# Optimization experiments

Hardware: AMD Instinct MI355X
Metric: run time of the kernel (lower is better)

The kernel has to match this reference:

```python
import jax, jax.numpy as jnp
import numpy as np

B, L, H = 4, 2048, 1024
NQ, NKV, D = 8, 2, 256
I, V = 3584, 16384
EPS = 1e-6
THETA = 1e7
ROPE_DIM = 64

def rmsnorm(x, w, eps=EPS):
    xf = x.astype(jnp.float32)
    rms = jax.lax.rsqrt(jnp.mean(xf * xf, axis=-1, keepdims=True) + eps)
    return (xf * rms).astype(x.dtype) * w

def apply_rope(x, positions):
    # x: [B, H, L, D]; rotate first ROPE_DIM dims, interleaved pairs
    n_pairs = ROPE_DIM // 2
    inv_freq = THETA ** (-2.0 * jnp.arange(n_pairs, dtype=jnp.float32) / ROPE_DIM)
    freqs = positions.astype(jnp.float32)[:, None] * inv_freq[None, :]  # [L, n_pairs]
    cos = jnp.cos(freqs)[None, None, :, :]
    sin = jnp.sin(freqs)[None, None, :, :]
    b, h, l, d = x.shape
    xr = x[..., :ROPE_DIM].reshape(b, h, l, n_pairs, 2)
    x0, x1 = xr[..., 0], xr[..., 1]
    r0 = x0 * cos - x1 * sin
    r1 = x0 * sin + x1 * cos
    rotated = jnp.stack([r0, r1], axis=-1).reshape(b, h, l, ROPE_DIM)
    return jnp.concatenate([rotated, x[..., ROPE_DIM:]], axis=-1)

def setup_inputs() -> dict:
    key = jax.random.key(0)
    ks = jax.random.split(key, 12)
    s = 0.02
    return {
        "embeddings": jax.random.normal(ks[0], (B, L, H), jnp.float32),
        "hidden_states": jax.random.normal(ks[1], (B, L, H), jnp.float32),
        "pre_emb_w": jnp.ones((H,), jnp.float32),
        "pre_hid_w": jnp.ones((H,), jnp.float32),
        "fc_w": jax.random.normal(ks[2], (H, 2 * H), jnp.float32) * s,
        "in_ln_w": jnp.ones((H,), jnp.float32),
        "q_w": jax.random.normal(ks[3], (2 * NQ * D, H), jnp.float32) * s,
        "k_w": jax.random.normal(ks[4], (NKV * D, H), jnp.float32) * s,
        "v_w": jax.random.normal(ks[5], (NKV * D, H), jnp.float32) * s,
        "o_w": jax.random.normal(ks[6], (H, NQ * D), jnp.float32) * s,
        "qn_w": jnp.ones((D,), jnp.float32),
        "kn_w": jnp.ones((D,), jnp.float32),
        "post_ln_w": jnp.ones((H,), jnp.float32),
        "gate_w": jax.random.normal(ks[7], (I, H), jnp.float32) * s,
        "up_w": jax.random.normal(ks[8], (I, H), jnp.float32) * s,
        "down_w": jax.random.normal(ks[9], (H, I), jnp.float32) * s,
        "norm_w": jnp.ones((H,), jnp.float32),
        "lm_w": jax.random.normal(ks[10], (V, H), jnp.float32) * s,
    }

def _attention(x, q_w, k_w, v_w, o_w, qn_w, kn_w):
    b, l, _ = x.shape
    qg = (x @ q_w.T).reshape(b, l, NQ, 2, D)
    q = qg[:, :, :, 0, :]
    gate = qg[:, :, :, 1, :]
    k = (x @ k_w.T).reshape(b, l, NKV, D)
    v = (x @ v_w.T).reshape(b, l, NKV, D)
    q = rmsnorm(q, qn_w)
    k = rmsnorm(k, kn_w)
    groups = NQ // NKV
    k = jnp.repeat(k, groups, axis=2)  # [B, L, NQ, D]
    v = jnp.repeat(v, groups, axis=2)
    q, k, v = (t.transpose(0, 2, 1, 3) for t in (q, k, v))  # [B, NQ, L, D]
    positions = jnp.arange(l)
    q = apply_rope(q, positions)
    k = apply_rope(k, positions)
    scores = jnp.einsum('bhqd,bhkd->bhqk', q, k) / jnp.sqrt(jnp.float32(D))
    causal = jnp.tril(jnp.ones((l, l), jnp.bool_))
    scores = jnp.where(causal[None, None], scores, jnp.finfo(scores.dtype).min)
    attn = jax.nn.softmax(scores, axis=-1)
    out = jnp.einsum('bhqk,bhkd->bhqd', attn, v)
    out = out.transpose(0, 2, 1, 3).reshape(b, l, NQ * D)
    out = out * jax.nn.sigmoid(gate.reshape(b, l, NQ * D))
    return out @ o_w.T

def reference(embeddings, hidden_states, pre_emb_w, pre_hid_w, fc_w, in_ln_w,
              q_w, k_w, v_w, o_w, qn_w, kn_w, post_ln_w, gate_w, up_w, down_w,
              norm_w, lm_w):
    x = jnp.concatenate([rmsnorm(embeddings, pre_emb_w),
                         rmsnorm(hidden_states, pre_hid_w)], axis=-1)
    x = x @ fc_w.T
    residual = x
    x = rmsnorm(x, in_ln_w)
    x = _attention(x, q_w, k_w, v_w, o_w, qn_w, kn_w)
    x = residual + x
    residual = x
    x = rmsnorm(x, post_ln_w)
    x = (jax.nn.silu(x @ gate_w.T) * (x @ up_w.T)) @ down_w.T
    x = residual + x
    x = rmsnorm(x, norm_w)
    return x @ lm_w.T
```

## Files before the change

### kernel.cpp

```cpp
#include <hip/hip_runtime.h>

typedef __bf16 bf16;
typedef __bf16 bf16x8 __attribute__((ext_vector_type(8)));
typedef __bf16 bf16x4 __attribute__((ext_vector_type(4)));
typedef float f32x4 __attribute__((ext_vector_type(4)));

__device__ inline f32x4 mfma16(bf16x8 a, bf16x8 b, f32x4 c) {
    return __builtin_amdgcn_mfma_f32_16x16x32_bf16(a, b, c, 0, 0, 0);
}

__device__ __forceinline__ void async_cp16(const void* g, void* l) {
    __builtin_amdgcn_global_load_lds(
        (__attribute__((address_space(1))) char*)g,
        (__attribute__((address_space(3))) char*)l,
        16, 0, 0);
}

__global__ __launch_bounds__(256) void w2b_kernel(const float* __restrict__ s,
                                                  bf16* __restrict__ d)
{
    const size_t i = ((size_t)blockIdx.x * 256 + threadIdx.x) * 4;
    const float4 f = *(const float4*)(s + i);
    bf16x4 t;
    t[0] = (bf16)f.x; t[1] = (bf16)f.y; t[2] = (bf16)f.z; t[3] = (bf16)f.w;
    *(bf16x4*)(d + i) = t;
}

template <int EPI>
__global__ __launch_bounds__(256) void gemm_kernel(
    const bf16* __restrict__ A, const bf16* __restrict__ B,
    const float* __restrict__ res, float* __restrict__ Cout,
    int M, int N, int K)
{
    __shared__ bf16 As[128 * 32];
    __shared__ bf16 Bs[128 * 32];
    const int tid = threadIdx.x;
    const int wave = tid >> 6, lane = tid & 63;
    const int quad = lane >> 4, l16 = lane & 15;

    const int nby = M >> 7, nbx = N >> 7;
    const int nwg = nbx * nby;
    int bid = blockIdx.x;
    {
        const int q = nwg >> 3, r = nwg & 7;
        const int x = bid & 7, loc = bid >> 3;
        bid = (x < r ? x * (q + 1) : r * (q + 1) + (x - r) * q) + loc;
    }
    const int pg = nbx << 3;
    const int g = bid / pg, rem = bid - g * pg;
    const int by = (g << 3) + (rem & 7);
    const int bx = rem >> 3;
    const int row0 = by << 7, col0 = bx << 7;
    const int wrow = ((wave >> 1) << 6), wcol = ((wave & 1) << 6);

    f32x4 acc[4][4] = {};

    const bf16* Ag = A + (size_t)(row0 + (tid >> 2)) * K + (tid & 3) * 8;
    const bf16* Bg = B + (size_t)(col0 + (tid >> 2)) * K + (tid & 3) * 8;
    bf16* Asw = As + wave * 512;
    bf16* Bsw = Bs + wave * 512;
    const size_t K64 = (size_t)64 * K;

    for (int kb = 0; kb < K; kb += 32) {
        async_cp16(Ag + kb,        Asw);
        async_cp16(Ag + K64 + kb,  Asw + 2048);
        async_cp16(Bg + kb,        Bsw);
        async_cp16(Bg + K64 + kb,  Bsw + 2048);
        __syncthreads();
        bf16x8 af[4], bfr[4];
#pragma unroll
        for (int i = 0; i < 4; ++i)
            af[i] = *(const bf16x8*)(&As[(wrow + i * 16 + l16) * 32 + quad * 8]);
#pragma unroll
        for (int j = 0; j < 4; ++j)
            bfr[j] = *(const bf16x8*)(&Bs[(wcol + j * 16 + l16) * 32 + quad * 8]);
#pragma unroll
        for (int i = 0; i < 4; ++i)
#pragma unroll
            for (int j = 0; j < 4; ++j)
                acc[i][j] = mfma16(af[i], bfr[j], acc[i][j]);
        __syncthreads();
    }

#pragma unroll
    for (int i = 0; i < 4; ++i) {
        const int row = row0 + wrow + i * 16 + quad * 4;
#pragma unroll
        for (int j = 0; j < 4; ++j) {
            const int col = col0 + wcol + j * 16 + l16;
#pragma unroll
            for (int r = 0; r < 4; ++r) {
                const size_t idx = (size_t)(row + r) * N + col;
                float v = acc[i][j][r];
                if (EPI == 1) Cout[idx] = v + res[idx];
                else          Cout[idx] = v;
            }
        }
    }
}

template <int EPI>
__global__ __launch_bounds__(512, 2) void gemm256_kernel(
    const bf16* __restrict__ A, const bf16* __restrict__ B,
    const float* __restrict__ res, float* __restrict__ Cout,
    int M, int N, int K)
{
    __shared__ bf16 As[2][2][128][64];
    __shared__ bf16 Bs[2][2][128][64];
    const int tid = threadIdx.x;
    const int wid = tid >> 6, lane = tid & 63;
    const int quad = lane >> 4, l16 = lane & 15;
    const int wm = wid >> 2, wn = wid & 3;
    const int xsw = l16 & 7;

    const int nby = M >> 8, nbx = N >> 8;
    const int nwg = nbx * nby;
    int bid = blockIdx.x;
    {
        const int q = nwg >> 3, r = nwg & 7;
        const int x = bid & 7, loc = bid >> 3;
        bid = (x < r ? x * (q + 1) : r * (q + 1) + (x - r) * q) + loc;
    }
    const int pg = nbx << 3;
    const int g = bid / pg, rem = bid - g * pg;
    const int by = (g << 3) + (rem & 7);
    const int bx = rem >> 3;
    const int row0 = by << 8, col0 = bx << 8;

    const int srow = tid >> 3;
    const int scol = ((tid & 7) ^ ((tid >> 3) & 7)) * 8;
    const bf16* Abase = A + (size_t)(row0 + srow) * K + scol;
    const bf16* Bbase = B + (size_t)(col0 + srow) * K + scol;
    const size_t K64 = (size_t)K * 64;
    const size_t K128 = (size_t)K * 128;

    f32x4 acc[8][4] = {};

#define STG_A(BUF, HH, KB) do { \
    const bf16* _g = Abase + (size_t)(HH) * K128 + (KB); \
    bf16* _l = &As[BUF][HH][0][0] + wid * 512; \
    async_cp16(_g, _l); \
    async_cp16(_g + K64, _l + 4096); } while (0)
#define STG_B(BUF, HH, KB) do { \
    const bf16* _g = Bbase + (size_t)(HH) * K128 + (KB); \
    bf16* _l = &Bs[BUF][HH][0][0] + wid * 512; \
    async_cp16(_g, _l); \
    async_cp16(_g + K64, _l + 4096); } while (0)

#define READ_A(RH) do { \
    _Pragma("unroll") for (int f = 0; f < 4; ++f) { \
        af[f*2+0] = *(const bf16x8*)(&Ah[(RH)*64 + f*16 + l16][(quad ^ xsw) * 8]); \
        af[f*2+1] = *(const bf16x8*)(&Ah[(RH)*64 + f*16 + l16][((4 + quad) ^ xsw) * 8]); } } while (0)

#define READ_B(CH, BF) do { \
    _Pragma("unroll") for (int f = 0; f < 2; ++f) { \
        BF[f*2+0] = *(const bf16x8*)(&Bh[bofs + (CH)*32 + f*16 + l16][(quad ^ xsw) * 8]); \
        BF[f*2+1] = *(const bf16x8*)(&Bh[bofs + (CH)*32 + f*16 + l16][((4 + quad) ^ xsw) * 8]); } } while (0)

#define MFMA_Q(RH, CH, BF) do { \
    _Pragma("unroll") for (int f = 0; f < 4; ++f) \
    _Pragma("unroll") for (int f2 = 0; f2 < 2; ++f2) { \
        acc[(RH)*4+f][(CH)*2+f2] = mfma16(af[f*2+0], BF[f2*2+0], acc[(RH)*4+f][(CH)*2+f2]); \
        acc[(RH)*4+f][(CH)*2+f2] = mfma16(af[f*2+1], BF[f2*2+1], acc[(RH)*4+f][(CH)*2+f2]); } } while (0)

    const int NT = K >> 6;
    STG_B(0, 0, 0); STG_B(0, 1, 0); STG_A(0, 0, 0); STG_A(0, 1, 0);
    if (NT > 1) {
        STG_B(1, 0, 64); STG_B(1, 1, 64); STG_A(1, 0, 64);
        asm volatile("s_waitcnt vmcnt(6)" ::: "memory");
    } else {
        asm volatile("s_waitcnt vmcnt(0)" ::: "memory");
    }
    __builtin_amdgcn_s_barrier();

    bf16x8 af[8], bf0[4], bf1[4];
    for (int t = 0; t < NT; ++t) {
        const int c = t & 1, n = c ^ 1;
        const bf16 (*Ah)[64] = As[c][wm];
        const bf16 (*Bh)[64] = Bs[c][wn >> 1];
        const int bofs = (wn & 1) * 64;
        const int kb1 = (t + 1) << 6, kb2 = (t + 2) << 6;
        READ_A(0); READ_B(0, bf0);
        if (t + 1 < NT) STG_A(n, 1, kb1);
        __builtin_amdgcn_s_barrier();
        asm volatile("s_waitcnt lgkmcnt(0)" ::: "memory");
        __builtin_amdgcn_sched_barrier(0);
        __builtin_amdgcn_s_setprio(1);
        MFMA_Q(0, 0, bf0);
        __builtin_amdgcn_s_setprio(0);
        __builtin_amdgcn_s_barrier();
        READ_B(1, bf1);
        if (t + 2 < NT) STG_B(c, 0, kb2);
        __builtin_amdgcn_s_barrier();
        asm volatile("s_waitcnt lgkmcnt(0)" ::: "memory");
        __builtin_amdgcn_sched_barrier(0);
        __builtin_amdgcn_s_setprio(1);
        MFMA_Q(0, 1, bf1);
        __builtin_amdgcn_s_setprio(0);
        __builtin_amdgcn_s_barrier();
        READ_A(1);
        if (t + 2 < NT) STG_B(c, 1, kb2);
        __builtin_amdgcn_s_barrier();
        asm volatile("s_waitcnt lgkmcnt(0)" ::: "memory");
        __builtin_amdgcn_sched_barrier(0);
        __builtin_amdgcn_s_setprio(1);
        MFMA_Q(1, 0, bf0);
        __builtin_amdgcn_s_setprio(0);
        __builtin_amdgcn_s_barrier();
        if (t + 2 < NT) STG_A(c, 0, kb2);
        __builtin_amdgcn_s_barrier();
        __builtin_amdgcn_s_setprio(1);
        MFMA_Q(1, 1, bf1);
        __builtin_amdgcn_s_setprio(0);
        if (t + 2 < NT)      { asm volatile("s_waitcnt vmcnt(6)" ::: "memory"); }
        else if (t + 1 < NT) { asm volatile("s_waitcnt vmcnt(0)" ::: "memory"); }
        __builtin_amdgcn_s_barrier();
    }
#undef STG_A
#undef STG_B
#undef READ_A
#undef READ_B
#undef MFMA_Q

#pragma unroll
    for (int fr = 0; fr < 8; ++fr) {
        const int row = row0 + wm * 128 + fr * 16 + quad * 4;
#pragma unroll
        for (int fc = 0; fc < 4; ++fc) {
            const int col = col0 + wn * 64 + fc * 16 + l16;
#pragma unroll
            for (int r = 0; r < 4; ++r) {
                const size_t idx = (size_t)(row + r) * N + col;
                float v = acc[fr][fc][r];
                if (EPI == 1) Cout[idx] = v + res[idx];
                else          Cout[idx] = v;
            }
        }
    }
}

__global__ __launch_bounds__(256) void prenorm_kernel(
    const float* __restrict__ emb, const float* __restrict__ hid,
    const float* __restrict__ we, const float* __restrict__ wh,
    bf16* __restrict__ xcat)
{
    const int rr = blockIdx.x * 4 + (threadIdx.x >> 6);
    const int lane = threadIdx.x & 63;
    const int half = rr & 1, row = rr >> 1;
    const float* x = (half ? hid : emb) + (size_t)row * 1024;
    const float* w = half ? wh : we;
    float4 v[4]; float ss = 0.f;
#pragma unroll
    for (int j = 0; j < 4; ++j) {
        v[j] = *(const float4*)(x + (size_t)(lane + 64 * j) * 4);
        ss += v[j].x * v[j].x + v[j].y * v[j].y + v[j].z * v[j].z + v[j].w * v[j].w;
    }
#pragma unroll
    for (int m = 32; m; m >>= 1) ss += __shfl_xor(ss, m, 64);
    const float rms = rsqrtf(ss * (1.f / 1024.f) + 1e-6f);
    bf16* o = xcat + (size_t)row * 2048 + half * 1024;
#pragma unroll
    for (int j = 0; j < 4; ++j) {
        const int d = (lane + 64 * j) * 4;
        float4 wv = *(const float4*)(w + d);
        bf16x4 t;
        t[0] = (bf16)(v[j].x * rms * wv.x);
        t[1] = (bf16)(v[j].y * rms * wv.y);
        t[2] = (bf16)(v[j].z * rms * wv.z);
        t[3] = (bf16)(v[j].w * rms * wv.w);
        *(bf16x4*)(o + d) = t;
    }
}

__global__ __launch_bounds__(256) void rmsnorm_kernel(
    const float* __restrict__ xin, const float* __restrict__ w, bf16* __restrict__ out)
{
    const int row = blockIdx.x * 4 + (threadIdx.x >> 6);
    const int lane = threadIdx.x & 63;
    const float* x = xin + (size_t)row * 1024;
    float4 v[4]; float ss = 0.f;
#pragma unroll
    for (int j = 0; j < 4; ++j) {
        v[j] = *(const float4*)(x + (size_t)(lane + 64 * j) * 4);
        ss += v[j].x * v[j].x + v[j].y * v[j].y + v[j].z * v[j].z + v[j].w * v[j].w;
    }
#pragma unroll
    for (int m = 32; m; m >>= 1) ss += __shfl_xor(ss, m, 64);
    const float rms = rsqrtf(ss * (1.f / 1024.f) + 1e-6f);
    bf16* o = out + (size_t)row * 1024;
#pragma unroll
    for (int j = 0; j < 4; ++j) {
        const int d = (lane + 64 * j) * 4;
        float4 wv = *(const float4*)(w + d);
        bf16x4 t;
        t[0] = (bf16)(v[j].x * rms * wv.x);
        t[1] = (bf16)(v[j].y * rms * wv.y);
        t[2] = (bf16)(v[j].z * rms * wv.z);
        t[3] = (bf16)(v[j].w * rms * wv.w);
        *(bf16x4*)(o + d) = t;
    }
}

__global__ __launch_bounds__(256) void qprep_kernel(
    const float* __restrict__ qg, const float* __restrict__ qn_w, bf16* __restrict__ qa)
{
    const int row = blockIdx.x * 4 + (threadIdx.x >> 6);
    const int lane = threadIdx.x & 63;
    const int h = row & 7, bl = row >> 3;
    const int l = bl & 2047, b = bl >> 11;
    const float* x = qg + (size_t)row * 512;
    float v[4]; float ss = 0.f;
#pragma unroll
    for (int j = 0; j < 4; ++j) { v[j] = x[lane + 64 * j]; ss += v[j] * v[j]; }
#pragma unroll
    for (int m = 32; m; m >>= 1) ss += __shfl_xor(ss, m, 64);
    const float rms = rsqrtf(ss * (1.f / 256.f) + 1e-6f);
    float y[4];
#pragma unroll
    for (int j = 0; j < 4; ++j) y[j] = v[j] * rms * qn_w[lane + 64 * j];
    {
        const float p = __shfl_xor(y[0], 1, 64);
        const int i2 = lane >> 1;
        const float inv = powf(1e7f, -(float)(2 * i2) * (1.f / 64.f));
        const float ang = (float)l * inv;
        const float c = cosf(ang), s = sinf(ang);
        y[0] = (lane & 1) ? (p * s + y[0] * c) : (y[0] * c - p * s);
    }
    bf16* o = qa + ((size_t)((b * 8 + h) * 2048 + l)) * 256;
#pragma unroll
    for (int j = 0; j < 4; ++j) o[lane + 64 * j] = (bf16)(y[j] * 0.0625f);
}

__global__ __launch_bounds__(256) void kprep_kernel(
    const float* __restrict__ kf, const float* __restrict__ kn_w, bf16* __restrict__ ka)
{
    const int row = blockIdx.x * 4 + (threadIdx.x >> 6);
    const int lane = threadIdx.x & 63;
    const int kv = row & 1, bl = row >> 1;
    const int l = bl & 2047, b = bl >> 11;
    const float* x = kf + (size_t)row * 256;
    float v[4]; float ss = 0.f;
#pragma unroll
    for (int j = 0; j < 4; ++j) { v[j] = x[lane + 64 * j]; ss += v[j] * v[j]; }
#pragma unroll
    for (int m = 32; m; m >>= 1) ss += __shfl_xor(ss, m, 64);
    const float rms = rsqrtf(ss * (1.f / 256.f) + 1e-6f);
    float y[4];
#pragma unroll
    for (int j = 0; j < 4; ++j) y[j] = v[j] * rms * kn_w[lane + 64 * j];
    {
        const float p = __shfl_xor(y[0], 1, 64);
        const int i2 = lane >> 1;
        const float inv = powf(1e7f, -(float)(2 * i2) * (1.f / 64.f));
        const float ang = (float)l * inv;
        const float c = cosf(ang), s = sinf(ang);
        y[0] = (lane & 1) ? (p * s + y[0] * c) : (y[0] * c - p * s);
    }
    bf16* o = ka + ((size_t)((b * 2 + kv) * 2048 + l)) * 256;
#pragma unroll
    for (int j = 0; j < 4; ++j) o[lane + 64 * j] = (bf16)y[j];
}

__global__ __launch_bounds__(256) void vprep_kernel(const float* __restrict__ vf,
                                                    bf16* __restrict__ vt)
{
    __shared__ float t[64][65];
    const int l0 = blockIdx.x << 6;
    const int d0 = blockIdx.y << 6;
    const int b = blockIdx.z >> 1, kv = blockIdx.z & 1;
    const int tx = threadIdx.x & 63, ty = threadIdx.x >> 6;
    const float* src = vf + ((size_t)b * 4096 + kv) * 256;
#pragma unroll
    for (int j = 0; j < 16; ++j) {
        const int l = ty + j * 4;
        t[l][tx] = src[(size_t)(l0 + l) * 512 + d0 + tx];
    }
    __syncthreads();
    bf16* dst = vt + (size_t)(b * 2 + kv) * 256 * 2048;
#pragma unroll
    for (int j = 0; j < 16; ++j) {
        const int d = ty + j * 4;
        dst[(size_t)(d0 + d) * 2048 + l0 + tx] = (bf16)t[tx][d];
    }
}

__global__ __launch_bounds__(256) void attn_kernel(
    const bf16* __restrict__ qa, const bf16* __restrict__ ka,
    const bf16* __restrict__ vt, float* __restrict__ of)
{
    __shared__ bf16 Ks[32 * 264];
    __shared__ bf16 Vt[256 * 40];
    __shared__ bf16 Pw[4 * 16 * 40];
    const int tid = threadIdx.x;
    const int wave = tid >> 6, lane = tid & 63;
    const int quad = lane >> 4, l16 = lane & 15;
    const int bid = blockIdx.x;
    const int j = bid & 15, h = (bid >> 4) & 7, b = bid >> 7;
    const int kvh = h >> 2;
    const bf16* qptr = qa + ((size_t)(b * 8 + h)) * 2048 * 256;
    const bf16* kptr = ka + ((size_t)(b * 2 + kvh)) * 2048 * 256;
    const bf16* vptr = vt + ((size_t)(b * 2 + kvh)) * 256 * 2048;
    float* optr = of + ((size_t)(b * 8 + h)) * 2048 * 256;

    for (int s = 0; s < 2; ++s) {
        const int qt = s ? (31 - j) : j;
        const int qbase = qt * 64 + wave * 16;

        bf16x8 qf[8];
#pragma unroll
        for (int db = 0; db < 8; ++db)
            qf[db] = *(const bf16x8*)(qptr + (size_t)(qbase + l16) * 256 + db * 32 + quad * 8);

        f32x4 o_acc[16] = {};
        float m_i[4], l_i[4];
#pragma unroll
        for (int r = 0; r < 4; ++r) { m_i[r] = -1e30f; l_i[r] = 0.f; }

        const int ntiles = qt * 2 + 2;
        for (int kt = 0; kt < ntiles; ++kt) {
            const int kvs = kt * 32;
#pragma unroll
            for (int c = 0; c < 4; ++c) {
                const int idx = tid + c * 256;
                const int kr = idx >> 5, kc = (idx & 31) * 8;
                *(bf16x8*)(&Ks[kr * 264 + kc]) = *(const bf16x8*)(kptr + (size_t)(kvs + kr) * 256 + kc);
                const int vd = idx >> 2, vc = (idx & 3) * 8;
                *(bf16x8*)(&Vt[vd * 40 + vc]) = *(const bf16x8*)(vptr + (size_t)vd * 2048 + kvs + vc);
            }
            __syncthreads();

            f32x4 s0 = {}, s1 = {};
#pragma unroll
            for (int db = 0; db < 8; ++db) {
                bf16x8 k0 = *(const bf16x8*)(&Ks[l16 * 264 + db * 32 + quad * 8]);
                bf16x8 k1 = *(const bf16x8*)(&Ks[(16 + l16) * 264 + db * 32 + quad * 8]);
                s0 = mfma16(qf[db], k0, s0);
                s1 = mfma16(qf[db], k1, s1);
            }

            float alpha[4], p0v[4], p1v[4];
#pragma unroll
            for (int r = 0; r < 4; ++r) {
                const int qrow = qbase + quad * 4 + r;
                float a0 = (kvs + l16 > qrow) ? -1e30f : s0[r];
                float a1 = (kvs + 16 + l16 > qrow) ? -1e30f : s1[r];
                float mx = fmaxf(a0, a1);
#pragma unroll
                for (int m = 8; m; m >>= 1) mx = fmaxf(mx, __shfl_xor(mx, m, 64));
                const float mnew = fmaxf(m_i[r], mx);
                const float a = __expf(m_i[r] - mnew);
                const float p0 = __expf(a0 - mnew);
                const float p1 = __expf(a1 - mnew);
                float ps = p0 + p1;
#pragma unroll
                for (int m = 8; m; m >>= 1) ps += __shfl_xor(ps, m, 64);
                l_i[r] = l_i[r] * a + ps;
                m_i[r] = mnew;
                alpha[r] = a; p0v[r] = p0; p1v[r] = p1;
            }
#pragma unroll
            for (int t = 0; t < 16; ++t) {
                f32x4 o = o_acc[t];
                o[0] *= alpha[0]; o[1] *= alpha[1]; o[2] *= alpha[2]; o[3] *= alpha[3];
                o_acc[t] = o;
            }
            bf16* pw = &Pw[wave * 16 * 40];
#pragma unroll
            for (int r = 0; r < 4; ++r) {
                pw[(quad * 4 + r) * 40 + l16]      = (bf16)p0v[r];
                pw[(quad * 4 + r) * 40 + 16 + l16] = (bf16)p1v[r];
            }
            __syncthreads();
            const bf16x8 pa = *(const bf16x8*)(&pw[l16 * 40 + quad * 8]);
#pragma unroll
            for (int t = 0; t < 16; ++t) {
                bf16x8 vfr = *(const bf16x8*)(&Vt[(t * 16 + l16) * 40 + quad * 8]);
                o_acc[t] = mfma16(pa, vfr, o_acc[t]);
            }
            __syncthreads();
        }

#pragma unroll
        for (int r = 0; r < 4; ++r) {
            const float inv = 1.f / l_i[r];
            const int row = qbase + quad * 4 + r;
#pragma unroll
            for (int t = 0; t < 16; ++t)
                optr[(size_t)row * 256 + t * 16 + l16] = o_acc[t][r] * inv;
        }
    }
}

__global__ void gating_kernel(const float* __restrict__ of, const float* __restrict__ qg,
                              bf16* __restrict__ ag)
{
    const size_t i = (size_t)blockIdx.x * 256 + threadIdx.x;
    const int d = (int)(i & 255);
    const int h = (int)((i >> 8) & 7);
    const size_t bl = i >> 11;
    const float o = of[((size_t)((bl >> 11) * 8 + h) * 2048 + (bl & 2047)) * 256 + d];
    const float g = qg[(bl * 8 + h) * 512 + 256 + d];
    ag[i] = (bf16)(o * (1.f / (1.f + __expf(-g))));
}

__global__ void silu_kernel(const float* __restrict__ g, const float* __restrict__ u,
                            bf16* __restrict__ h)
{
    const size_t i = ((size_t)blockIdx.x * 256 + threadIdx.x) * 4;
    const float4 gv = *(const float4*)(g + i);
    const float4 uv = *(const float4*)(u + i);
    bf16x4 t;
    t[0] = (bf16)(gv.x * (1.f / (1.f + __expf(-gv.x))) * uv.x);
    t[1] = (bf16)(gv.y * (1.f / (1.f + __expf(-gv.y))) * uv.y);
    t[2] = (bf16)(gv.z * (1.f / (1.f + __expf(-gv.z))) * uv.z);
    t[3] = (bf16)(gv.w * (1.f / (1.f + __expf(-gv.w))) * uv.w);
    *(bf16x4*)(h + i) = t;
}

extern "C" void kernel_launch(void* const* d_in, const int* in_sizes, int n_in,
                              void* d_out, int out_size, void* d_ws, size_t ws_size,
                              hipStream_t stream)
{
    const float* emb       = (const float*)d_in[0];
    const float* hid       = (const float*)d_in[1];
    const float* pre_emb_w = (const float*)d_in[2];
    const float* pre_hid_w = (const float*)d_in[3];
    const float* fc_w      = (const float*)d_in[4];
    const float* in_ln_w   = (const float*)d_in[5];
    const float* q_w       = (const float*)d_in[6];
    const float* k_w       = (const float*)d_in[7];
    const float* v_w       = (const float*)d_in[8];
    const float* o_w       = (const float*)d_in[9];
    const float* qn_w      = (const float*)d_in[10];
    const float* kn_w      = (const float*)d_in[11];
    const float* post_ln_w = (const float*)d_in[12];
    const float* gate_w    = (const float*)d_in[13];
    const float* up_w      = (const float*)d_in[14];
    const float* down_w    = (const float*)d_in[15];
    const float* norm_w    = (const float*)d_in[16];
    const float* lm_w      = (const float*)d_in[17];
    float* out = (float*)d_out;
    char* ws = (char*)d_ws;

    float* xres = (float*)(ws + 0);
    bf16*  xln  = (bf16*)(ws + 33554432);
    char*  C    = ws + 50331648;
    char*  D    = ws + 184549376;
    char*  E    = ws + 318767104;
    float* qg   = (float*)C;
    float* gf   = (float*)C;
    bf16*  xcat = (bf16*)D;
    float* kf   = (float*)(D + 33554432);
    float* vf   = (float*)(D + 50331648);
    float* of   = (float*)(D + 67108864);
    float* uf   = (float*)D;
    bf16*  qa   = (bf16*)E;
    bf16*  ka   = (bf16*)(E + 33554432);
    bf16*  va   = (bf16*)(E + 41943040);
    bf16*  ag   = (bf16*)E;
    bf16*  hb   = (bf16*)E;
    bf16*  wbC  = (bf16*)C;
    bf16*  wbD  = (bf16*)D;
    bf16*  wbDt = (bf16*)(D + 117440512);

    prenorm_kernel<<<4096, 256, 0, stream>>>(emb, hid, pre_emb_w, pre_hid_w, xcat);

    w2b_kernel<<<2048, 256, 0, stream>>>(fc_w, wbC);
    gemm_kernel<0><<<512, 256, 0, stream>>>(xcat, wbC, nullptr, xres, 8192, 1024, 2048);
    rmsnorm_kernel<<<2048, 256, 0, stream>>>(xres, in_ln_w, xln);

    w2b_kernel<<<4096, 256, 0, stream>>>(q_w, wbD);
    gemm256_kernel<0><<<512, 512, 0, stream>>>(xln, wbD, nullptr, qg, 8192, 4096, 1024);
    w2b_kernel<<<512, 256, 0, stream>>>(k_w, wbD);
    gemm_kernel<0><<<256, 256, 0, stream>>>(xln, wbD, nullptr, kf, 8192, 512, 1024);
    w2b_kernel<<<512, 256, 0, stream>>>(v_w, wbD);
    gemm_kernel<0><<<256, 256, 0, stream>>>(xln, wbD, nullptr, vf, 8192, 512, 1024);

    qprep_kernel<<<16384, 256, 0, stream>>>(qg, qn_w, qa);
    kprep_kernel<<<4096, 256, 0, stream>>>(kf, kn_w, ka);
    vprep_kernel<<<dim3(32, 4, 8), 256, 0, stream>>>(vf, va);
    attn_kernel<<<512, 256, 0, stream>>>(qa, ka, va, of);
    gating_kernel<<<65536, 256, 0, stream>>>(of, qg, ag);

    w2b_kernel<<<2048, 256, 0, stream>>>(o_w, wbC);
    gemm_kernel<1><<<512, 256, 0, stream>>>(ag, wbC, xres, xres, 8192, 1024, 2048);
    rmsnorm_kernel<<<2048, 256, 0, stream>>>(xres, post_ln_w, xln);

    w2b_kernel<<<3584, 256, 0, stream>>>(gate_w, wbDt);
    gemm256_kernel<0><<<448, 512, 0, stream>>>(xln, wbDt, nullptr, gf, 8192, 3584, 1024);
    w2b_kernel<<<3584, 256, 0, stream>>>(up_w, wbDt);
    gemm256_kernel<0><<<448, 512, 0, stream>>>(xln, wbDt, nullptr, uf, 8192, 3584, 1024);
    silu_kernel<<<28672, 256, 0, stream>>>(gf, uf, hb);

    w2b_kernel<<<3584, 256, 0, stream>>>(down_w, wbC);
    gemm_kernel<1><<<512, 256, 0, stream>>>(hb, wbC, xres, xres, 8192, 1024, 3584);
    rmsnorm_kernel<<<2048, 256, 0, stream>>>(xres, norm_w, xln);

    w2b_kernel<<<16384, 256, 0, stream>>>(lm_w, wbC);
    gemm256_kernel<0><<<2048, 512, 0, stream>>>(xln, wbC, nullptr, out, 8192, 16384, 1024);
}
```

Baseline: 1.880 ms.

## Prefetch next K/V tile into registers in attention and reschedule GEMM B reads

The attention kernel now loads the next K/V tile from global memory into registers while the current tile's QK and PV MFMAs run, then writes it to LDS after the tile finishes. This hides global load latency behind compute. The 256-tile GEMM now reads the first B fragment for the next k-step at the end of the current iteration and groups both B staging copies into one slot, changing how LDS reads and async copies overlap. The cost is higher register pressure in attention (8 extra bf16x8 per thread) and a changed LDS hazard ordering in the GEMM.

```diff
diff --git a/kernel.cpp b/kernel.cpp
--- a/kernel.cpp
+++ b/kernel.cpp
@@ -112,6 +112,7 @@
     const int quad = lane >> 4, l16 = lane & 15;
     const int wm = wid >> 2, wn = wid & 3;
     const int xsw = l16 & 7;
+    const int bofs = (wn & 1) * 64;
 
     const int nby = M >> 8, nbx = N >> 8;
     const int nwg = nbx * nby;
@@ -152,10 +153,10 @@
         af[f*2+0] = *(const bf16x8*)(&Ah[(RH)*64 + f*16 + l16][(quad ^ xsw) * 8]); \
         af[f*2+1] = *(const bf16x8*)(&Ah[(RH)*64 + f*16 + l16][((4 + quad) ^ xsw) * 8]); } } while (0)
 
-#define READ_B(CH, BF) do { \
+#define READ_Bp(BP, CH, BF) do { \
     _Pragma("unroll") for (int f = 0; f < 2; ++f) { \
-        BF[f*2+0] = *(const bf16x8*)(&Bh[bofs + (CH)*32 + f*16 + l16][(quad ^ xsw) * 8]); \
-        BF[f*2+1] = *(const bf16x8*)(&Bh[bofs + (CH)*32 + f*16 + l16][((4 + quad) ^ xsw) * 8]); } } while (0)
+        BF[f*2+0] = *(const bf16x8*)(&BP[bofs + (CH)*32 + f*16 + l16][(quad ^ xsw) * 8]); \
+        BF[f*2+1] = *(const bf16x8*)(&BP[bofs + (CH)*32 + f*16 + l16][((4 + quad) ^ xsw) * 8]); } } while (0)
 
 #define MFMA_Q(RH, CH, BF) do { \
     _Pragma("unroll") for (int f = 0; f < 4; ++f) \
@@ -174,13 +175,16 @@
     __builtin_amdgcn_s_barrier();
 
     bf16x8 af[8], bf0[4], bf1[4];
+    {
+        const bf16 (*Bh0)[64] = Bs[0][wn >> 1];
+        READ_Bp(Bh0, 0, bf0);
+    }
     for (int t = 0; t < NT; ++t) {
         const int c = t & 1, n = c ^ 1;
         const bf16 (*Ah)[64] = As[c][wm];
         const bf16 (*Bh)[64] = Bs[c][wn >> 1];
-        const int bofs = (wn & 1) * 64;
         const int kb1 = (t + 1) << 6, kb2 = (t + 2) << 6;
-        READ_A(0); READ_B(0, bf0);
+        READ_A(0);
         if (t + 1 < NT) STG_A(n, 1, kb1);
         __builtin_amdgcn_s_barrier();
         asm volatile("s_waitcnt lgkmcnt(0)" ::: "memory");
@@ -189,8 +193,7 @@
         MFMA_Q(0, 0, bf0);
         __builtin_amdgcn_s_setprio(0);
         __builtin_amdgcn_s_barrier();
-        READ_B(1, bf1);
-        if (t + 2 < NT) STG_B(c, 0, kb2);
+        READ_Bp(Bh, 1, bf1);
         __builtin_amdgcn_s_barrier();
         asm volatile("s_waitcnt lgkmcnt(0)" ::: "memory");
         __builtin_amdgcn_sched_barrier(0);
@@ -199,7 +202,7 @@
         __builtin_amdgcn_s_setprio(0);
         __builtin_amdgcn_s_barrier();
         READ_A(1);
-        if (t + 2 < NT) STG_B(c, 1, kb2);
+        if (t + 2 < NT) { STG_B(c, 0, kb2); STG_B(c, 1, kb2); }
         __builtin_amdgcn_s_barrier();
         asm volatile("s_waitcnt lgkmcnt(0)" ::: "memory");
         __builtin_amdgcn_sched_barrier(0);
@@ -214,12 +217,16 @@
         __builtin_amdgcn_s_setprio(0);
         if (t + 2 < NT)      { asm volatile("s_waitcnt vmcnt(6)" ::: "memory"); }
         else if (t + 1 < NT) { asm volatile("s_waitcnt vmcnt(0)" ::: "memory"); }
+        if (t + 1 < NT) {
+            const bf16 (*Bn_)[64] = Bs[n][wn >> 1];
+            READ_Bp(Bn_, 0, bf0);
+        }
         __builtin_amdgcn_s_barrier();
     }
 #undef STG_A
 #undef STG_B
 #undef READ_A
-#undef READ_B
+#undef READ_Bp
 #undef MFMA_Q
 
 #pragma unroll
@@ -417,17 +424,31 @@
         for (int r = 0; r < 4; ++r) { m_i[r] = -1e30f; l_i[r] = 0.f; }
 
         const int ntiles = qt * 2 + 2;
+#pragma unroll
+        for (int c = 0; c < 4; ++c) {
+            const int idx = tid + c * 256;
+            const int kr = idx >> 5, kc = (idx & 31) * 8;
+            *(bf16x8*)(&Ks[kr * 264 + kc]) = *(const bf16x8*)(kptr + (size_t)kr * 256 + kc);
+            const int vd = idx >> 2, vc = (idx & 3) * 8;
+            *(bf16x8*)(&Vt[vd * 40 + vc]) = *(const bf16x8*)(vptr + (size_t)vd * 2048 + vc);
+        }
+        __syncthreads();
+
         for (int kt = 0; kt < ntiles; ++kt) {
             const int kvs = kt * 32;
-#pragma unroll
-            for (int c = 0; c < 4; ++c) {
-                const int idx = tid + c * 256;
-                const int kr = idx >> 5, kc = (idx & 31) * 8;
-                *(bf16x8*)(&Ks[kr * 264 + kc]) = *(const bf16x8*)(kptr + (size_t)(kvs + kr) * 256 + kc);
-                const int vd = idx >> 2, vc = (idx & 3) * 8;
-                *(bf16x8*)(&Vt[vd * 40 + vc]) = *(const bf16x8*)(vptr + (size_t)vd * 2048 + kvs + vc);
-            }
-            __syncthreads();
+            const bool pf = (kt + 1 < ntiles);
+            bf16x8 kreg[4], vreg[4];
+            if (pf) {
+                const int kvs1 = kvs + 32;
+#pragma unroll
+                for (int c = 0; c < 4; ++c) {
+                    const int idx = tid + c * 256;
+                    const int kr = idx >> 5, kc = (idx & 31) * 8;
+                    kreg[c] = *(const bf16x8*)(kptr + (size_t)(kvs1 + kr) * 256 + kc);
+                    const int vd = idx >> 2, vc = (idx & 3) * 8;
+                    vreg[c] = *(const bf16x8*)(vptr + (size_t)vd * 2048 + kvs1 + vc);
+                }
+            }
 
             f32x4 s0 = {}, s1 = {};
 #pragma unroll
@@ -478,6 +499,18 @@
                 o_acc[t] = mfma16(pa, vfr, o_acc[t]);
             }
             __syncthreads();
+
+            if (pf) {
+#pragma unroll
+                for (int c = 0; c < 4; ++c) {
+                    const int idx = tid + c * 256;
+                    const int kr = idx >> 5, kc = (idx & 31) * 8;
+                    *(bf16x8*)(&Ks[kr * 264 + kc]) = kreg[c];
+                    const int vd = idx >> 2, vc = (idx & 3) * 8;
+                    *(bf16x8*)(&Vt[vd * 40 + vc]) = vreg[c];
+                }
+                __syncthreads();
+            }
         }
 
 #pragma unroll
```

After: 1.921 ms. 2.2% more time.

## Restructure GEMM main loop to prefetch next tile's LDS fragments and cut barriers

Applied to the files above, without the earlier changes.

The 256x256 bf16 GEMM main loop is rescheduled. The A fragments and both B fragment sets for the next K-tile are now read from LDS at the end of the current iteration, so the next iteration's MFMAs can start right away. Global-to-LDS staging is regrouped: both A halves are staged early and both B halves after the mid-iteration barrier. This cuts the workgroup barriers per K-step from about eight to two and uses partial lgkmcnt/vmcnt waits. The aim is to reduce barrier stalls and LDS latency exposure between MFMA batches, at the cost of more live fragment registers and a tighter buffer-reuse ordering that must stay race-free.

```diff
diff --git a/kernel.cpp b/kernel.cpp
--- a/kernel.cpp
+++ b/kernel.cpp
@@ -112,6 +112,7 @@
     const int quad = lane >> 4, l16 = lane & 15;
     const int wm = wid >> 2, wn = wid & 3;
     const int xsw = l16 & 7;
+    const int bofs = (wn & 1) * 64;
 
     const int nby = M >> 8, nbx = N >> 8;
     const int nwg = nbx * nby;
@@ -135,6 +136,7 @@
     const size_t K128 = (size_t)K * 128;
 
     f32x4 acc[8][4] = {};
+    bf16x8 af[8], bf0[4], bf1[4];
 
 #define STG_A(BUF, HH, KB) do { \
     const bf16* _g = Abase + (size_t)(HH) * K128 + (KB); \
@@ -147,15 +149,17 @@
     async_cp16(_g, _l); \
     async_cp16(_g + K64, _l + 4096); } while (0)
 
-#define READ_A(RH) do { \
+#define RD_A(BUF, RH) do { \
+    const bf16 (*Ah_)[64] = As[BUF][wm]; \
     _Pragma("unroll") for (int f = 0; f < 4; ++f) { \
-        af[f*2+0] = *(const bf16x8*)(&Ah[(RH)*64 + f*16 + l16][(quad ^ xsw) * 8]); \
-        af[f*2+1] = *(const bf16x8*)(&Ah[(RH)*64 + f*16 + l16][((4 + quad) ^ xsw) * 8]); } } while (0)
-
-#define READ_B(CH, BF) do { \
+        af[f*2+0] = *(const bf16x8*)(&Ah_[(RH)*64 + f*16 + l16][(quad ^ xsw) * 8]); \
+        af[f*2+1] = *(const bf16x8*)(&Ah_[(RH)*64 + f*16 + l16][((4 + quad) ^ xsw) * 8]); } } while (0)
+
+#define RD_B(BUF, CH, BF) do { \
+    const bf16 (*Bh_)[64] = Bs[BUF][wn >> 1]; \
     _Pragma("unroll") for (int f = 0; f < 2; ++f) { \
-        BF[f*2+0] = *(const bf16x8*)(&Bh[bofs + (CH)*32 + f*16 + l16][(quad ^ xsw) * 8]); \
-        BF[f*2+1] = *(const bf16x8*)(&Bh[bofs + (CH)*32 + f*16 + l16][((4 + quad) ^ xsw) * 8]); } } while (0)
+        BF[f*2+0] = *(const bf16x8*)(&Bh_[bofs + (CH)*32 + f*16 + l16][(quad ^ xsw) * 8]); \
+        BF[f*2+1] = *(const bf16x8*)(&Bh_[bofs + (CH)*32 + f*16 + l16][((4 + quad) ^ xsw) * 8]); } } while (0)
 
 #define MFMA_Q(RH, CH, BF) do { \
     _Pragma("unroll") for (int f = 0; f < 4; ++f) \
@@ -164,62 +168,55 @@
         acc[(RH)*4+f][(CH)*2+f2] = mfma16(af[f*2+1], BF[f2*2+1], acc[(RH)*4+f][(CH)*2+f2]); } } while (0)
 
     const int NT = K >> 6;
-    STG_B(0, 0, 0); STG_B(0, 1, 0); STG_A(0, 0, 0); STG_A(0, 1, 0);
+    STG_A(0, 0, 0); STG_A(0, 1, 0); STG_B(0, 0, 0); STG_B(0, 1, 0);
     if (NT > 1) {
-        STG_B(1, 0, 64); STG_B(1, 1, 64); STG_A(1, 0, 64);
-        asm volatile("s_waitcnt vmcnt(6)" ::: "memory");
+        STG_A(1, 0, 64); STG_A(1, 1, 64); STG_B(1, 0, 64); STG_B(1, 1, 64);
+        asm volatile("s_waitcnt vmcnt(8)" ::: "memory");
     } else {
         asm volatile("s_waitcnt vmcnt(0)" ::: "memory");
     }
+    __builtin_amdgcn_sched_barrier(0);
     __builtin_amdgcn_s_barrier();
-
-    bf16x8 af[8], bf0[4], bf1[4];
+    RD_A(0, 0); RD_B(0, 0, bf0); RD_B(0, 1, bf1);
+    __builtin_amdgcn_sched_barrier(0);
+
     for (int t = 0; t < NT; ++t) {
         const int c = t & 1, n = c ^ 1;
-        const bf16 (*Ah)[64] = As[c][wm];
-        const bf16 (*Bh)[64] = Bs[c][wn >> 1];
-        const int bofs = (wn & 1) * 64;
         const int kb1 = (t + 1) << 6, kb2 = (t + 2) << 6;
-        READ_A(0); READ_B(0, bf0);
-        if (t + 1 < NT) STG_A(n, 1, kb1);
-        __builtin_amdgcn_s_barrier();
-        asm volatile("s_waitcnt lgkmcnt(0)" ::: "memory");
+        if (t >= 1 && t + 1 < NT) { STG_A(n, 0, kb1); STG_A(n, 1, kb1); }
+        asm volatile("s_waitcnt lgkmcnt(4)" ::: "memory");
         __builtin_amdgcn_sched_barrier(0);
         __builtin_amdgcn_s_setprio(1);
         MFMA_Q(0, 0, bf0);
         __builtin_amdgcn_s_setprio(0);
-        __builtin_amdgcn_s_barrier();
-        READ_B(1, bf1);
-        if (t + 2 < NT) STG_B(c, 0, kb2);
-        __builtin_amdgcn_s_barrier();
         asm volatile("s_waitcnt lgkmcnt(0)" ::: "memory");
         __builtin_amdgcn_sched_barrier(0);
         __builtin_amdgcn_s_setprio(1);
         MFMA_Q(0, 1, bf1);
         __builtin_amdgcn_s_setprio(0);
+        RD_A(c, 1);
+        __builtin_amdgcn_sched_barrier(0);
         __builtin_amdgcn_s_barrier();
-        READ_A(1);
-        if (t + 2 < NT) STG_B(c, 1, kb2);
-        __builtin_amdgcn_s_barrier();
+        if (t + 2 < NT) { STG_B(c, 0, kb2); STG_B(c, 1, kb2); }
         asm volatile("s_waitcnt lgkmcnt(0)" ::: "memory");
         __builtin_amdgcn_sched_barrier(0);
         __builtin_amdgcn_s_setprio(1);
         MFMA_Q(1, 0, bf0);
-        __builtin_amdgcn_s_setprio(0);
-        __builtin_amdgcn_s_barrier();
-        if (t + 2 < NT) STG_A(c, 0, kb2);
-        __builtin_amdgcn_s_barrier();
-        __builtin_amdgcn_s_setprio(1);
         MFMA_Q(1, 1, bf1);
         __builtin_amdgcn_s_setprio(0);
-        if (t + 2 < NT)      { asm volatile("s_waitcnt vmcnt(6)" ::: "memory"); }
-        else if (t + 1 < NT) { asm volatile("s_waitcnt vmcnt(0)" ::: "memory"); }
+        if (t + 1 < NT) {
+            if (t + 2 < NT) { asm volatile("s_waitcnt vmcnt(4)" ::: "memory"); }
+            else            { asm volatile("s_waitcnt vmcnt(0)" ::: "memory"); }
+            __builtin_amdgcn_sched_barrier(0);
+            RD_A(n, 0); RD_B(n, 0, bf0); RD_B(n, 1, bf1);
+            __builtin_amdgcn_sched_barrier(0);
+        }
         __builtin_amdgcn_s_barrier();
     }
 #undef STG_A
 #undef STG_B
-#undef READ_A
-#undef READ_B
+#undef RD_A
+#undef RD_B
 #undef MFMA_Q
 
 #pragma unroll
```

Result: no change. 1.858 ms (-1.2%).
